# Kernel tuning notes

Measured on AMD Instinct MI355X. Metric: run time of the kernel, lower is better.

The kernel has to match this reference:

```python
import jax, jax.numpy as jnp
import numpy as np

EMBED = 768
N_HEADS = 12
HEAD = EMBED // N_HEADS  # 64
B, T = 2, 2048


def setup_inputs() -> dict:
    key = jax.random.key(0)
    ks = jax.random.split(key, 5)
    s = 0.02
    return {
        "x": jax.random.normal(ks[0], (B, T, EMBED), dtype=jnp.float32),
        "w_attn": jax.random.normal(ks[1], (EMBED, 3 * EMBED), dtype=jnp.float32) * s,
        "b_attn": jnp.zeros((3 * EMBED,), dtype=jnp.float32),
        "w_proj": jax.random.normal(ks[2], (EMBED, EMBED), dtype=jnp.float32) * s,
        "b_proj": jnp.zeros((EMBED,), dtype=jnp.float32),
    }


def reference(x, w_attn, b_attn, w_proj, b_proj):
    b, t, c = x.shape
    scale = HEAD ** -0.5
    qkv = x @ w_attn + b_attn  # [b,t,3c]
    q, k, v = jnp.split(qkv, 3, axis=-1)

    # einops 'b t (h n) -> b n t h' with n=N_HEADS: channel dim factors as
    # (head_size, n_heads) — head index is the inner factor.
    def split_heads(u):
        return u.reshape(b, t, HEAD, N_HEADS).transpose(0, 3, 1, 2)  # [b,n,t,h]

    q, k, v = split_heads(q), split_heads(k), split_heads(v)

    scores = jnp.einsum("bnth,bnsh->bnts", q, k) * scale  # [b,n,t,t]
    causal = jnp.tril(jnp.ones((t, t), dtype=bool))
    scores = jnp.where(causal, scores, jnp.finfo(scores.dtype).min)
    weights = jax.nn.softmax(scores, axis=-1)
    att = jnp.einsum("bnts,bnsh->bnth", weights, v)  # [b,n,t,h]

    # 'b n t h -> b t (n h)': heads are the OUTER factor on output
    att = att.transpose(0, 2, 1, 3).reshape(b, t, c)
    return att @ w_proj + b_proj
```

## Files before the change

kernel.cpp:

```cpp
#include <hip/hip_runtime.h>
#include <hip/hip_bf16.h>
#include <math.h>

#define NB      2
#define T_SZ    2048
#define EMBEDC  768
#define NHEADS  12
#define HEADD   64
#define QKV_PER (NB * NHEADS * T_SZ * HEADD)
#define QSCALE  0.18033688011112042f

typedef __bf16 bf16x8 __attribute__((ext_vector_type(8)));
typedef float  f32x4  __attribute__((ext_vector_type(4)));

__device__ inline ushort f2bf(float x) {
    union { float f; uint u; } v; v.f = x;
    uint r = v.u + 0x7fffu + ((v.u >> 16) & 1u);
    return (ushort)(r >> 16);
}

__device__ inline uint pack2bf(float a, float b) {
    union { __bf16 h[2]; uint u; } t;
    t.h[0] = (__bf16)a; t.h[1] = (__bf16)b;
    return t.u;
}

__device__ inline void gload16(const ushort* g, ushort* l) {
    __builtin_amdgcn_global_load_lds(
        (const __attribute__((address_space(1))) unsigned int*)g,
        (__attribute__((address_space(3))) unsigned int*)l, 16, 0, 0);
}

__global__ __launch_bounds__(256) void cast_k(const float* __restrict__ in,
                                              ushort* __restrict__ out, int n)
{
    int i = (blockIdx.x * 256 + threadIdx.x) * 8;
    if (i >= n) return;
    float4 a = *(const float4*)(in + i);
    float4 b = *(const float4*)(in + i + 4);
    union { ushort u[8]; int4 v; } p;
    p.u[0] = f2bf(a.x); p.u[1] = f2bf(a.y); p.u[2] = f2bf(a.z); p.u[3] = f2bf(a.w);
    p.u[4] = f2bf(b.x); p.u[5] = f2bf(b.y); p.u[6] = f2bf(b.z); p.u[7] = f2bf(b.w);
    *(int4*)(out + i) = p.v;
}

template <int PERM>
__global__ __launch_bounds__(256) void tcast_k(const float* __restrict__ in,
                                               ushort* __restrict__ out,
                                               int R, int C)
{
    __shared__ float t[32][33];
    const int c0 = blockIdx.x * 32, r0 = blockIdx.y * 32;
    const int tx = threadIdx.x & 31, ty = threadIdx.x >> 5;
#pragma unroll
    for (int u = 0; u < 4; ++u)
        t[ty + 8 * u][tx] = in[(size_t)(r0 + ty + 8 * u) * C + c0 + tx];
    __syncthreads();
#pragma unroll
    for (int u = 0; u < 4; ++u) {
        int n = c0 + ty + 8 * u;
        int orow = n;
        if (PERM) {
            int mat = n / EMBEDC, cc = n % EMBEDC;
            orow = mat * EMBEDC + (cc % NHEADS) * HEADD + cc / NHEADS;
        }
        out[(size_t)orow * R + r0 + tx] = f2bf(t[tx][ty + 8 * u]);
    }
}

__global__ __launch_bounds__(256) void vt_k(const ushort* __restrict__ in,
                                            ushort* __restrict__ out)
{
    __shared__ ushort tile[64][66];
    const int bh = blockIdx.y;
    const int t0 = blockIdx.x * 64;
    const int tid = threadIdx.x;
#pragma unroll
    for (int u = 0; u < 2; ++u) {
        int s = tid + 256 * u;
        int r = s >> 3, c8 = s & 7;
        *(bf16x8*)&tile[r][c8 * 8] =
            *(const bf16x8*)(in + ((size_t)bh * T_SZ + t0 + r) * HEADD + c8 * 8);
    }
    __syncthreads();
#pragma unroll
    for (int u = 0; u < 2; ++u) {
        int s = tid + 256 * u;
        int hd = s >> 3, tt = s & 7;
        union { ushort v[8]; int4 q; } pk;
#pragma unroll
        for (int j = 0; j < 8; ++j) pk.v[j] = tile[tt * 8 + j][hd];
        *(int4*)(out + ((size_t)bh * HEADD + hd) * T_SZ + t0 + tt * 8) = pk.q;
    }
}

#define STAGE(buf, koff)                                        \
    do {                                                        \
        gload16(gA0 + (koff), &As[buf][lA0o]);                  \
        gload16(gA1 + (koff), &As[buf][lA1o]);                  \
        gload16(gB0 + (koff), &Bs[buf][lB0o]);                  \
        gload16(gB1 + (koff), &Bs[buf][lB1o]);                  \
    } while (0)

template <int MODE>
__global__ __launch_bounds__(256) void gemm_bf16_k(
    const ushort* __restrict__ A, const ushort* __restrict__ Bt,
    const float* __restrict__ bias, void* __restrict__ outp,
    int M, int N, int K)
{
    __shared__ ushort As[2][128 * 32];
    __shared__ ushort Bs[2][128 * 32];

    const int tid = threadIdx.x;
    const int w = tid >> 6, l = tid & 63;
    const int g = l >> 4, r16 = l & 15;
    const int wr = w >> 1, wc = w & 1;
    const int m0 = blockIdx.y * 128, n0 = blockIdx.x * 128;

    const int srow = l >> 2;
    const int scol = ((l & 3) ^ (srow & 3)) * 8;
    const ushort* gA0 = A + (size_t)(m0 + 32 * w + srow) * K + scol;
    const ushort* gA1 = gA0 + (size_t)16 * K;
    const ushort* gB0 = Bt + (size_t)(n0 + 32 * w + srow) * K + scol;
    const ushort* gB1 = gB0 + (size_t)16 * K;
    const int lA0o = (32 * w) * 32,      lA1o = (32 * w + 16) * 32;
    const int lB0o = lA0o,               lB1o = lA1o;

    f32x4 acc[4][4];
#pragma unroll
    for (int i = 0; i < 4; ++i)
#pragma unroll
        for (int j = 0; j < 4; ++j) acc[i][j] = (f32x4){0.f, 0.f, 0.f, 0.f};

    const int rck = (r16 & 3);

    STAGE(0, 0);
    __syncthreads();

    int cur = 0;
    for (int k0 = 0; k0 < K; k0 += 32) {
        if (k0 + 32 < K) STAGE(cur ^ 1, k0 + 32);

        const ushort* sA = As[cur];
        const ushort* sB = Bs[cur];
        bf16x8 af[4], bfr[4];
#pragma unroll
        for (int ms = 0; ms < 4; ++ms) {
            int row = 64 * wr + 16 * ms + r16;
            af[ms] = *(const bf16x8*)&sA[row * 32 + ((g ^ rck) * 8)];
        }
#pragma unroll
        for (int ns = 0; ns < 4; ++ns) {
            int row = 64 * wc + 16 * ns + r16;
            bfr[ns] = *(const bf16x8*)&sB[row * 32 + ((g ^ rck) * 8)];
        }
#pragma unroll
        for (int ms = 0; ms < 4; ++ms)
#pragma unroll
            for (int ns = 0; ns < 4; ++ns)
                acc[ms][ns] = __builtin_amdgcn_mfma_f32_16x16x32_bf16(
                    af[ms], bfr[ns], acc[ms][ns], 0, 0, 0);

        __syncthreads();
        cur ^= 1;
    }

#pragma unroll
    for (int ns = 0; ns < 4; ++ns) {
        const int n = n0 + 64 * wc + 16 * ns + r16;
        if (MODE == 0) {
            float* out = (float*)outp;
            const float bv = bias[n];
#pragma unroll
            for (int ms = 0; ms < 4; ++ms) {
                const int mb = m0 + 64 * wr + 16 * ms + 4 * g;
#pragma unroll
                for (int r = 0; r < 4; ++r)
                    out[(size_t)(mb + r) * N + n] = acc[ms][ns][r] + bv;
            }
        } else {
            ushort* ob = (ushort*)outp;
            const int mat  = n / EMBEDC;
            const int c    = n - mat * EMBEDC;
            const int head = c >> 6;
            const int hd   = c & 63;
            const float bv = bias[mat * EMBEDC + hd * NHEADS + head];
            const float qs = (mat == 0) ? QSCALE : 1.f;
#pragma unroll
            for (int ms = 0; ms < 4; ++ms) {
                const int mb = m0 + 64 * wr + 16 * ms + 4 * g;
#pragma unroll
                for (int r = 0; r < 4; ++r) {
                    const int m = mb + r;
                    const int b = m >> 11, t = m & 2047;
                    const size_t bh = (size_t)(b * NHEADS + head);
                    ob[(size_t)mat * QKV_PER + (bh * T_SZ + t) * HEADD + hd] =
                        f2bf((acc[ms][ns][r] + bv) * qs);
                }
            }
        }
    }
}

#define ASTAGE(k0)                                                            \
    do {                                                                      \
        _Pragma("unroll")                                                     \
        for (int u = 0; u < 4; ++u) {                                         \
            int s = tid + 256 * u;                                            \
            int krow = s >> 3, kc8 = s & 7;                                   \
            gload16(Kg + (size_t)((k0) + krow) * HEADD +                      \
                        ((kc8 ^ (krow & 7)) * 8),                             \
                    Ks + (64 * w + 256 * u) * 8);                             \
            int vrow = s >> 4, vc16 = s & 15;                                 \
            gload16(Vg + (size_t)vrow * T_SZ + (k0) +                         \
                        ((vc16 ^ (vrow & 15)) * 8),                           \
                    Vs + (64 * w + 256 * u) * 8);                             \
        }                                                                     \
    } while (0)

__global__ __launch_bounds__(256) void attn_mfma_k(
    const ushort* __restrict__ Qb, const ushort* __restrict__ Kb,
    const ushort* __restrict__ Vtb, ushort* __restrict__ Out)
{
    __shared__ ushort smem[16384];
    __shared__ float Ml[128], Ll[128];

    ushort* Ks = smem;
    ushort* Vs = smem + 8192;
    float*  fsm = (float*)smem;

    const int bh = blockIdx.x >> 5;
    const int p  = blockIdx.x & 31;
    const int bb = bh / NHEADS, head = bh % NHEADS;
    const int tid = threadIdx.x;
    const int w = tid >> 6, l = tid & 63;
    const int g = l >> 4, r16 = l & 15;
    const ushort* Qg = Qb + (size_t)bh * T_SZ * HEADD;
    const ushort* Kg = Kb + (size_t)bh * T_SZ * HEADD;
    const ushort* Vg = Vtb + (size_t)bh * HEADD * T_SZ;

    const int srcLo = ((g & 1) << 5) | r16;
    const int srcHi = srcLo + 16;
    const bool kcSel = (g >> 1) != 0;

    for (int rep = 0; rep < 2; ++rep) {
        const int iq = rep ? (63 - p) : p;
        const int q0 = iq * 32;
        const int qmax = q0 + 31;
        const int nt = iq / 4 + 1;

        bf16x8 qf[2][2];
#pragma unroll
        for (int qi = 0; qi < 2; ++qi) {
            const ushort* qp = Qg + (size_t)(q0 + qi * 16 + r16) * HEADD + g * 8;
            qf[qi][0] = *(const bf16x8*)(qp);
            qf[qi][1] = *(const bf16x8*)(qp + 32);
        }

        f32x4 o[4][2];
#pragma unroll
        for (int dc = 0; dc < 4; ++dc)
#pragma unroll
            for (int qi = 0; qi < 2; ++qi) o[dc][qi] = (f32x4){0.f, 0.f, 0.f, 0.f};
        float mR[2] = {-1e30f, -1e30f}, lR[2] = {0.f, 0.f};

        __syncthreads();
        ASTAGE(0);
        __syncthreads();

        for (int kt = 0; kt < nt; ++kt) {
            const int kvb = kt * 128 + 32 * w;
            const bool act = (kt + 1 < nt) || (kvb <= qmax);
            if (act) {
                f32x4 st[2][2];
#pragma unroll
                for (int kc = 0; kc < 2; ++kc) {
                    int row = 32 * w + kc * 16 + r16;
                    const ushort* kp = &Ks[row * 64];
                    bf16x8 a0 = *(const bf16x8*)(kp + ((g    ) ^ (r16 & 7)) * 8);
                    bf16x8 a1 = *(const bf16x8*)(kp + ((g + 4) ^ (r16 & 7)) * 8);
#pragma unroll
                    for (int qi = 0; qi < 2; ++qi) {
                        f32x4 c = (f32x4){0.f, 0.f, 0.f, 0.f};
                        c = __builtin_amdgcn_mfma_f32_16x16x32_bf16(a0, qf[qi][0], c, 0, 0, 0);
                        c = __builtin_amdgcn_mfma_f32_16x16x32_bf16(a1, qf[qi][1], c, 0, 0, 0);
                        st[kc][qi] = c;
                    }
                }

                if (kt == nt - 1) {
#pragma unroll
                    for (int kc = 0; kc < 2; ++kc)
#pragma unroll
                        for (int qi = 0; qi < 2; ++qi)
#pragma unroll
                            for (int r = 0; r < 4; ++r)
                                if (kvb + kc * 16 + 4 * g + r > q0 + qi * 16 + r16)
                                    st[kc][qi][r] = -1e30f;
                }

                float pm[2];
#pragma unroll
                for (int qi = 0; qi < 2; ++qi) {
                    float m = fmaxf(fmaxf(st[0][qi][0], st[0][qi][1]),
                                    fmaxf(st[0][qi][2], st[0][qi][3]));
                    m = fmaxf(m, fmaxf(fmaxf(st[1][qi][0], st[1][qi][1]),
                                       fmaxf(st[1][qi][2], st[1][qi][3])));
                    m = fmaxf(m, __shfl_xor(m, 16));
                    m = fmaxf(m, __shfl_xor(m, 32));
                    pm[qi] = m;
                }
                float dm = fmaxf(pm[0] - mR[0], pm[1] - mR[1]);
                if (!__all(dm <= 8.f)) {
#pragma unroll
                    for (int qi = 0; qi < 2; ++qi) {
                        float mNew = fmaxf(mR[qi], pm[qi]);
                        float sc = exp2f(mR[qi] - mNew);
                        lR[qi] *= sc;
                        mR[qi] = mNew;
#pragma unroll
                        for (int dc = 0; dc < 4; ++dc) o[dc][qi] *= sc;
                    }
                }
#pragma unroll
                for (int qi = 0; qi < 2; ++qi) {
                    float rs = 0.f;
#pragma unroll
                    for (int kc = 0; kc < 2; ++kc)
#pragma unroll
                        for (int r = 0; r < 4; ++r) {
                            float e = exp2f(st[kc][qi][r] - mR[qi]);
                            st[kc][qi][r] = e;
                            rs += e;
                        }
                    rs += __shfl_xor(rs, 16);
                    rs += __shfl_xor(rs, 32);
                    lR[qi] += rs;
                }

                uint pk[2][2][2];
#pragma unroll
                for (int qi = 0; qi < 2; ++qi)
#pragma unroll
                    for (int kc = 0; kc < 2; ++kc) {
                        pk[qi][kc][0] = pack2bf(st[kc][qi][0], st[kc][qi][1]);
                        pk[qi][kc][1] = pack2bf(st[kc][qi][2], st[kc][qi][3]);
                    }

                bf16x8 vf[4];
#pragma unroll
                for (int dc = 0; dc < 4; ++dc) {
                    int row = dc * 16 + r16;
                    vf[dc] = *(const bf16x8*)
                        &Vs[row * 128 + (((4 * w + g) ^ r16) * 8)];
                }

#pragma unroll
                for (int qi = 0; qi < 2; ++qi) {
                    uint A0 = (uint)__shfl((int)pk[qi][0][0], srcLo);
                    uint A1 = (uint)__shfl((int)pk[qi][0][1], srcLo);
                    uint B0 = (uint)__shfl((int)pk[qi][1][0], srcLo);
                    uint B1 = (uint)__shfl((int)pk[qi][1][1], srcLo);
                    uint A2 = (uint)__shfl((int)pk[qi][0][0], srcHi);
                    uint A3 = (uint)__shfl((int)pk[qi][0][1], srcHi);
                    uint B2 = (uint)__shfl((int)pk[qi][1][0], srcHi);
                    uint B3 = (uint)__shfl((int)pk[qi][1][1], srcHi);
                    union { uint u[4]; bf16x8 v; } t;
                    t.u[0] = kcSel ? B0 : A0;
                    t.u[1] = kcSel ? B1 : A1;
                    t.u[2] = kcSel ? B2 : A2;
                    t.u[3] = kcSel ? B3 : A3;
#pragma unroll
                    for (int dc = 0; dc < 4; ++dc)
                        o[dc][qi] = __builtin_amdgcn_mfma_f32_16x16x32_bf16(
                            vf[dc], t.v, o[dc][qi], 0, 0, 0);
                }
            }

            __syncthreads();
            if (kt + 1 < nt) {
                ASTAGE((kt + 1) * 128);
                __syncthreads();
            }
        }

        if (g == 0) {
#pragma unroll
            for (int qi = 0; qi < 2; ++qi) {
                Ml[w * 32 + qi * 16 + r16] = mR[qi];
                Ll[w * 32 + qi * 16 + r16] = lR[qi];
            }
        }
        __syncthreads();

        float lt[2];
#pragma unroll
        for (int qi = 0; qi < 2; ++qi) {
            const int ix = qi * 16 + r16;
            float m0 = Ml[ix], m1 = Ml[32 + ix], m2 = Ml[64 + ix], m3 = Ml[96 + ix];
            float mt = fmaxf(fmaxf(m0, m1), fmaxf(m2, m3));
            float f = exp2f(mR[qi] - mt);
#pragma unroll
            for (int dc = 0; dc < 4; ++dc) o[dc][qi] *= f;
            lt[qi] = Ll[ix]      * exp2f(m0 - mt) + Ll[32 + ix] * exp2f(m1 - mt)
                   + Ll[64 + ix] * exp2f(m2 - mt) + Ll[96 + ix] * exp2f(m3 - mt);
        }

#pragma unroll
        for (int dc = 0; dc < 4; ++dc)
#pragma unroll
            for (int qi = 0; qi < 2; ++qi)
                *(f32x4*)&fsm[w * 2048 + (qi * 16 + r16) * 64 +
                              (((dc * 4 + g) ^ r16) * 4)] = o[dc][qi];
        __syncthreads();

#pragma unroll
        for (int qi = 0; qi < 2; ++qi) {
            const int off = (qi * 16 + r16) * 64 + (((w * 4 + g) ^ r16) * 4);
            f32x4 a = *(const f32x4*)&fsm[off];
            a += *(const f32x4*)&fsm[2048 + off];
            a += *(const f32x4*)&fsm[4096 + off];
            a += *(const f32x4*)&fsm[6144 + off];
            const float inv = 1.f / lt[qi];
            ushort4 pv;
            pv.x = f2bf(a[0] * inv);
            pv.y = f2bf(a[1] * inv);
            pv.z = f2bf(a[2] * inv);
            pv.w = f2bf(a[3] * inv);
            *(ushort4*)(Out + ((size_t)(bb * T_SZ + q0 + qi * 16 + r16)) * EMBEDC
                        + head * HEADD + w * 16 + 4 * g) = pv;
        }
    }
}

extern "C" void kernel_launch(void* const* d_in, const int* in_sizes, int n_in,
                              void* d_out, int out_size, void* d_ws, size_t ws_size,
                              hipStream_t stream)
{
    const float* x      = (const float*)d_in[0];
    const float* w_attn = (const float*)d_in[1];
    const float* b_attn = (const float*)d_in[2];
    const float* w_proj = (const float*)d_in[3];
    const float* b_proj = (const float*)d_in[4];
    float* out = (float*)d_out;

    ushort* qw   = (ushort*)d_ws;
    ushort* vT   = qw + (size_t)3 * QKV_PER;
    ushort* attb = vT + QKV_PER;
    ushort* xb   = attb + QKV_PER;
    ushort* waT  = xb + QKV_PER;
    ushort* wpT  = waT + (size_t)EMBEDC * 3 * EMBEDC;

    cast_k<<<QKV_PER / (256 * 8), 256, 0, stream>>>(x, xb, QKV_PER);
    tcast_k<1><<<dim3(3 * EMBEDC / 32, EMBEDC / 32), 256, 0, stream>>>(
        w_attn, waT, EMBEDC, 3 * EMBEDC);
    tcast_k<0><<<dim3(EMBEDC / 32, EMBEDC / 32), 256, 0, stream>>>(
        w_proj, wpT, EMBEDC, EMBEDC);

    gemm_bf16_k<1><<<dim3(2304 / 128, 4096 / 128), 256, 0, stream>>>(
        xb, waT, b_attn, qw, NB * T_SZ, 3 * EMBEDC, EMBEDC);

    vt_k<<<dim3(T_SZ / 64, NB * NHEADS), 256, 0, stream>>>(
        qw + 2 * (size_t)QKV_PER, vT);

    attn_mfma_k<<<768, 256, 0, stream>>>(
        qw, qw + QKV_PER, vT, attb);

    gemm_bf16_k<0><<<dim3(768 / 128, 4096 / 128), 256, 0, stream>>>(
        attb, wpT, b_proj, out, NB * T_SZ, EMBEDC, EMBEDC);
}
```

Before: 127.1 us.

## Load K/V attention tiles directly into registers and remap blocks per XCD

The attention kernel stops staging K and V tiles through shared memory with block-wide barriers. Each wave now loads its own K and V fragments straight from global memory into registers and prefetches the next K tile while computing the current one. Shared memory is kept only for the final cross-wave reduction. Block indices are also remapped so that all blocks of a given batch-head land on the same XCD, which should improve L2 reuse. The trade-off is more global and L2 traffic with possibly uncoalesced per-lane loads and higher register pressure, in exchange for removing barrier stalls.

```diff
diff --git a/kernel.cpp b/kernel.cpp
--- a/kernel.cpp
+++ b/kernel.cpp
@@ -202,35 +202,17 @@
     }
 }
 
-#define ASTAGE(k0)                                                            \
-    do {                                                                      \
-        _Pragma("unroll")                                                     \
-        for (int u = 0; u < 4; ++u) {                                         \
-            int s = tid + 256 * u;                                            \
-            int krow = s >> 3, kc8 = s & 7;                                   \
-            gload16(Kg + (size_t)((k0) + krow) * HEADD +                      \
-                        ((kc8 ^ (krow & 7)) * 8),                             \
-                    Ks + (64 * w + 256 * u) * 8);                             \
-            int vrow = s >> 4, vc16 = s & 15;                                 \
-            gload16(Vg + (size_t)vrow * T_SZ + (k0) +                         \
-                        ((vc16 ^ (vrow & 15)) * 8),                           \
-                    Vs + (64 * w + 256 * u) * 8);                             \
-        }                                                                     \
-    } while (0)
-
 __global__ __launch_bounds__(256) void attn_mfma_k(
     const ushort* __restrict__ Qb, const ushort* __restrict__ Kb,
     const ushort* __restrict__ Vtb, ushort* __restrict__ Out)
 {
-    __shared__ ushort smem[16384];
+    __shared__ float fsm[4 * 2048];
     __shared__ float Ml[128], Ll[128];
 
-    ushort* Ks = smem;
-    ushort* Vs = smem + 8192;
-    float*  fsm = (float*)smem;
-
-    const int bh = blockIdx.x >> 5;
-    const int p  = blockIdx.x & 31;
+    const int bid = blockIdx.x;
+    const int xcd = bid & 7, j = bid >> 3;
+    const int bh = xcd * 3 + (j >> 5);
+    const int p  = j & 31;
     const int bb = bh / NHEADS, head = bh % NHEADS;
     const int tid = threadIdx.x;
     const int w = tid >> 6, l = tid & 63;
@@ -243,6 +225,18 @@
     const int srcHi = srcLo + 16;
     const bool kcSel = (g >> 1) != 0;
 
+    const ushort* Kw = Kg + (size_t)(32 * w + r16) * HEADD;
+    const ushort* Vw = Vg + (size_t)r16 * T_SZ + 32 * w + g * 8;
+
+#define LOADK(dst, k0)                                                        \
+    do {                                                                      \
+        _Pragma("unroll")                                                     \
+        for (int kc = 0; kc < 2; ++kc) {                                      \
+            dst[kc * 2 + 0] = *(const bf16x8*)(Kw + (size_t)((k0) + kc * 16) * HEADD + g * 8);        \
+            dst[kc * 2 + 1] = *(const bf16x8*)(Kw + (size_t)((k0) + kc * 16) * HEADD + (g + 4) * 8);  \
+        }                                                                     \
+    } while (0)
+
     for (int rep = 0; rep < 2; ++rep) {
         const int iq = rep ? (63 - p) : p;
         const int q0 = iq * 32;
@@ -264,29 +258,33 @@
             for (int qi = 0; qi < 2; ++qi) o[dc][qi] = (f32x4){0.f, 0.f, 0.f, 0.f};
         float mR[2] = {-1e30f, -1e30f}, lR[2] = {0.f, 0.f};
 
-        __syncthreads();
-        ASTAGE(0);
-        __syncthreads();
+        bf16x8 kc0[4];
+        LOADK(kc0, 0);
 
         for (int kt = 0; kt < nt; ++kt) {
-            const int kvb = kt * 128 + 32 * w;
-            const bool act = (kt + 1 < nt) || (kvb <= qmax);
-            if (act) {
+            const int k0 = kt * 128;
+            const int kvb = k0 + 32 * w;
+            if (kvb <= qmax) {
+                bf16x8 vf[4];
+#pragma unroll
+                for (int dc = 0; dc < 4; ++dc)
+                    vf[dc] = *(const bf16x8*)(Vw + (size_t)(dc * 16) * T_SZ + k0);
+
+                bf16x8 kn[4];
+                if (kt + 1 < nt) LOADK(kn, k0 + 128);
+
                 f32x4 st[2][2];
 #pragma unroll
-                for (int kc = 0; kc < 2; ++kc) {
-                    int row = 32 * w + kc * 16 + r16;
-                    const ushort* kp = &Ks[row * 64];
-                    bf16x8 a0 = *(const bf16x8*)(kp + ((g    ) ^ (r16 & 7)) * 8);
-                    bf16x8 a1 = *(const bf16x8*)(kp + ((g + 4) ^ (r16 & 7)) * 8);
+                for (int kc = 0; kc < 2; ++kc)
 #pragma unroll
                     for (int qi = 0; qi < 2; ++qi) {
                         f32x4 c = (f32x4){0.f, 0.f, 0.f, 0.f};
-                        c = __builtin_amdgcn_mfma_f32_16x16x32_bf16(a0, qf[qi][0], c, 0, 0, 0);
-                        c = __builtin_amdgcn_mfma_f32_16x16x32_bf16(a1, qf[qi][1], c, 0, 0, 0);
+                        c = __builtin_amdgcn_mfma_f32_16x16x32_bf16(
+                                kc0[kc * 2 + 0], qf[qi][0], c, 0, 0, 0);
+                        c = __builtin_amdgcn_mfma_f32_16x16x32_bf16(
+                                kc0[kc * 2 + 1], qf[qi][1], c, 0, 0, 0);
                         st[kc][qi] = c;
                     }
-                }
 
                 if (kt == nt - 1) {
 #pragma unroll
@@ -346,14 +344,6 @@
                         pk[qi][kc][0] = pack2bf(st[kc][qi][0], st[kc][qi][1]);
                         pk[qi][kc][1] = pack2bf(st[kc][qi][2], st[kc][qi][3]);
                     }
-
-                bf16x8 vf[4];
-#pragma unroll
-                for (int dc = 0; dc < 4; ++dc) {
-                    int row = dc * 16 + r16;
-                    vf[dc] = *(const bf16x8*)
-                        &Vs[row * 128 + (((4 * w + g) ^ r16) * 8)];
-                }
 
 #pragma unroll
                 for (int qi = 0; qi < 2; ++qi) {
@@ -375,15 +365,15 @@
                         o[dc][qi] = __builtin_amdgcn_mfma_f32_16x16x32_bf16(
                             vf[dc], t.v, o[dc][qi], 0, 0, 0);
                 }
+
+                if (kt + 1 < nt) {
+#pragma unroll
+                    for (int i = 0; i < 4; ++i) kc0[i] = kn[i];
+                }
             }
-
-            __syncthreads();
-            if (kt + 1 < nt) {
-                ASTAGE((kt + 1) * 128);
-                __syncthreads();
-            }
-        }
-
+        }
+
+        __syncthreads();
         if (g == 0) {
 #pragma unroll
             for (int qi = 0; qi < 2; ++qi) {
@@ -431,6 +421,7 @@
                         + head * HEADD + w * 16 + 4 * g) = pv;
         }
     }
+#undef LOADK
 }
 
 extern "C" void kernel_launch(void* const* d_in, const int* in_sizes, int n_in,
```

After: 120.4 us. 5.3% less time.
